# Kernel optimization log

Measured on AMD Instinct MI355X. Metric: run time of the kernel, lower is better.

Reference implementation:

```python
import jax, jax.numpy as jnp
import numpy as np

B, CIN, COUT, K, E, H, W = 32, 128, 256, 3, 8, 64, 64


def setup_inputs() -> dict:
    key = jax.random.key(0)
    k1, k2, k3, k4 = jax.random.split(key, 4)
    x = jax.random.normal(k1, (B, CIN, H, W), dtype=jnp.float32)
    expert_weight = jax.random.normal(k2, (E, COUT, CIN, K, K), dtype=jnp.float32)
    # nn.Linear(in_channels, num_experts): weight [E, CIN], bias [E]
    bound = 1.0 / np.sqrt(CIN)
    routing_w = jax.random.uniform(k3, (E, CIN), minval=-bound, maxval=bound, dtype=jnp.float32)
    routing_b = jax.random.uniform(k4, (E,), minval=-bound, maxval=bound, dtype=jnp.float32)
    return {"x": x, "expert_weight": expert_weight, "routing_w": routing_w, "routing_b": routing_b}


def reference(x, expert_weight, routing_w, routing_b):
    # routing: global-avg-pool -> linear -> softmax over experts
    pooled = x.mean(axis=(2, 3))                             # [B, CIN]
    logits = pooled @ routing_w.T + routing_b                # [B, E]
    rweights = jax.nn.softmax(logits, axis=-1)               # [B, E]
    # per-sample combined conv weights: [B, COUT, CIN, K, K]
    cw = jnp.einsum('be,eoikl->boikl', rweights, expert_weight)

    def conv_one(xi, wi):
        # xi: [CIN, H, W], wi: [COUT, CIN, K, K]; VALID conv, stride 1
        return jax.lax.conv_general_dilated(
            xi[None], wi, window_strides=(1, 1), padding='VALID',
            dimension_numbers=('NCHW', 'OIHW', 'NCHW'))[0]

    return jax.vmap(conv_one)(x, cw)                         # [B, COUT, H-K+1, W-K+1]
```

## Files before the change

### kernel.cpp

```cpp
#include <hip/hip_runtime.h>
#include <hip/hip_bf16.h>


#define CC_B    32
#define CC_CIN  128
#define CC_COUT 256
#define CC_NP   3844
#define CC_NT   18

typedef __attribute__((ext_vector_type(8))) short bf16x8;
typedef __attribute__((ext_vector_type(4))) float f32x4;

__global__ void cc_nhwc(const float* __restrict__ x, __hip_bfloat16* __restrict__ xn,
                        float* __restrict__ psum) {
    const int b = blockIdx.x >> 6, y = blockIdx.x & 63;
    __shared__ float lds[64 * 129];
    __shared__ float sred[256];
    const int t = threadIdx.x;
    const float* src = x + (size_t)b * CC_CIN * 4096 + y * 64;
#pragma unroll
    for (int i = 0; i < 32; ++i) {
        const int idx = i * 256 + t;
        const int cin = idx >> 6, xx = idx & 63;
        lds[xx * 129 + cin] = src[(size_t)cin * 4096 + xx];
    }
    __syncthreads();
    __hip_bfloat16* dst = xn + ((size_t)b * 4096 + y * 64) * CC_CIN;
#pragma unroll
    for (int j = 0; j < 4; ++j) {
        const int cidx = j * 256 + t;
        const int xx = cidx >> 4, c8 = (cidx & 15) * 8;
        union { __hip_bfloat16 h[8]; uint4 v; } u;
#pragma unroll
        for (int jj = 0; jj < 8; ++jj) u.h[jj] = __float2bfloat16(lds[xx * 129 + c8 + jj]);
        *reinterpret_cast<uint4*>(dst + (size_t)xx * CC_CIN + c8) = u.v;
    }
    const int cin = t & 127, xh = (t >> 7) * 32;
    float s = 0.f;
#pragma unroll
    for (int xx = 0; xx < 32; ++xx) s += lds[(xh + xx) * 129 + cin];
    sred[t] = s;
    __syncthreads();
    if (t < 128) psum[((size_t)b * 64 + y) * CC_CIN + t] = sred[t] + sred[t + 128];
}

__global__ void cc_route(const float* __restrict__ psum,
                         const float* __restrict__ rw_w,
                         const float* __restrict__ rw_b,
                         float* __restrict__ rweights) {
    const int b = blockIdx.x, c = threadIdx.x;
    __shared__ float pl[128];
    __shared__ float lg[8];
    const float* p = psum + (size_t)b * 64 * CC_CIN + c;
    float s = 0.f;
#pragma unroll 8
    for (int y = 0; y < 64; ++y) s += p[(size_t)y * CC_CIN];
    pl[c] = s * (1.f / 4096.f);
    __syncthreads();
    if (c < 8) {
        const float* w = rw_w + c * CC_CIN;
        float a = rw_b[c];
#pragma unroll 8
        for (int i = 0; i < CC_CIN; ++i) a += pl[i] * w[i];
        lg[c] = a;
    }
    __syncthreads();
    if (c == 0) {
        float m = lg[0];
#pragma unroll
        for (int e = 1; e < 8; ++e) m = fmaxf(m, lg[e]);
        float ex[8], sm = 0.f;
#pragma unroll
        for (int e = 0; e < 8; ++e) { ex[e] = __expf(lg[e] - m); sm += ex[e]; }
#pragma unroll
        for (int e = 0; e < 8; ++e) rweights[b * 8 + e] = ex[e] / sm;
    }
}

__global__ void cc_combine(const float* __restrict__ ew,
                           const float* __restrict__ rw,
                           __hip_bfloat16* __restrict__ cw) {
    const int t9 = blockIdx.x >> 8;
    const int cout = blockIdx.x & 255;
    const int cin = threadIdx.x;
    __shared__ float rws[256];
    rws[cin] = rw[cin];
    rws[cin + 128] = rw[cin + 128];
    __syncthreads();
    float wv[8];
    const size_t base = ((size_t)cout * CC_CIN + cin) * 9 + t9;
#pragma unroll
    for (int e = 0; e < 8; ++e) wv[e] = ew[base + (size_t)e * (CC_COUT * CC_CIN * 9)];
#pragma unroll 4
    for (int b = 0; b < CC_B; ++b) {
        float acc = 0.f;
#pragma unroll
        for (int e = 0; e < 8; ++e) acc += rws[b * 8 + e] * wv[e];
        cw[(((size_t)b * 9 + t9) * CC_COUT + cout) * CC_CIN + cin] = __float2bfloat16(acc);
    }
}

__device__ __forceinline__ void gload_lds16(const void* g, void* l) {
    __builtin_amdgcn_global_load_lds(
        (const __attribute__((address_space(1))) unsigned int*)g,
        (__attribute__((address_space(3))) unsigned int*)l, 16, 0, 0);
}

__global__ __launch_bounds__(512, 1) void cc_conv(
    const __hip_bfloat16* __restrict__ xn,
    const __hip_bfloat16* __restrict__ cw,
    float* __restrict__ out)
{
    __shared__ __align__(16) char smem[131072];
    const int l   = blockIdx.x;
    const int xcd = l & 7, li = l >> 3;
    const int b   = 4 * xcd + (li >> 5);
    const int r2  = li & 31;
    const int nt  = r2 >> 1, mt = r2 & 1;
    const int m0  = mt * 128;
    const int n0  = nt * 248;
    const int y0  = nt * 4;

    const int tid = threadIdx.x;
    const int wid = tid >> 6, lane = tid & 63;
    const int waveM = wid >> 2, waveN = wid & 3;

    f32x4 acc[4][4];
#pragma unroll
    for (int i = 0; i < 4; ++i)
#pragma unroll
        for (int j = 0; j < 4; ++j) acc[i][j] = (f32x4){0.f, 0.f, 0.f, 0.f};

    const int gsw = (lane & 7) ^ (lane >> 3);
    const __hip_bfloat16* cwb = cw + (size_t)b * 9 * CC_COUT * CC_CIN;
    const __hip_bfloat16* xnb = xn + (size_t)b * 4096 * CC_CIN;

    char* Bres = smem + 32768;
#pragma unroll
    for (int i = 0; i < 12; ++i) {
        const int idx = i * 8 + wid;
        const int h = idx / 48, rem = idx - h * 48;
        const int yy = rem >> 3, xb = rem & 7;
        const int x = xb * 8 + (lane >> 3);
        int yin = y0 + yy; if (yin > 63) yin = 63;
        gload_lds16(xnb + ((size_t)yin * 64 + x) * CC_CIN + h * 64 + gsw * 8,
                    Bres + idx * 1024);
    }

    int laOff[2];
#pragma unroll
    for (int i = 0; i < 2; ++i) {
        const int row = wid * 16 + i * 8 + (lane >> 3);
        laOff[i] = (m0 + row) * CC_CIN + gsw * 8;
    }
    auto stageA = [&](int t) {
        const int t9 = t >> 1;
        const int aoff = t9 * (CC_COUT * CC_CIN) + (t & 1) * 64;
        char* Ab = smem + (t & 1) * 16384 + wid * 2048;
#pragma unroll
        for (int i = 0; i < 2; ++i)
            gload_lds16(cwb + aoff + laOff[i], Ab + i * 1024);
    };
    stageA(0);
    stageA(1);

    const int rl = lane & 15, q = lane >> 4;
    int oyl[4], oxl[4];
#pragma unroll
    for (int nf = 0; nf < 4; ++nf) {
        int c = waveN * 64 + nf * 16 + rl;
        if (c > 247) c = 247;
        const int oy = c / 62;
        oyl[nf] = oy;
        oxl[nf] = c - 62 * oy;
    }

#pragma unroll 1
    for (int t = 0; t < CC_NT; ++t) {
        const char* Ab = smem + (t & 1) * 16384;
        const int t9 = t >> 1;
        const int ky = (t9 * 11) >> 5;
        const int kx = t9 - ky * 3;
        const int h = t & 1;

        if (t < CC_NT - 1) asm volatile("s_waitcnt vmcnt(2)" ::: "memory");
        else               asm volatile("s_waitcnt vmcnt(0)" ::: "memory");
        asm volatile("s_barrier" ::: "memory");

        bf16x8 af[8], bf[8];
#pragma unroll
        for (int mf = 0; mf < 4; ++mf)
#pragma unroll
            for (int kk = 0; kk < 2; ++kk) {
                const int r = waveM * 64 + mf * 16 + rl;
                af[mf * 2 + kk] = *(const bf16x8*)(Ab + r * 128 + (((kk * 4 + q) ^ (r & 7)) * 16));
            }
#pragma unroll
        for (int nf = 0; nf < 4; ++nf) {
            const int x = oxl[nf] + kx;
            const int row = (h * 6 + oyl[nf] + ky) * 64 + x;
#pragma unroll
            for (int kk = 0; kk < 2; ++kk)
                bf[nf * 2 + kk] = *(const bf16x8*)(Bres + row * 128 + (((kk * 4 + q) ^ (x & 7)) * 16));
        }
#pragma unroll
        for (int kk = 0; kk < 2; ++kk)
#pragma unroll
            for (int mf = 0; mf < 4; ++mf)
#pragma unroll
                for (int nf = 0; nf < 4; ++nf)
                    acc[mf][nf] = __builtin_amdgcn_mfma_f32_16x16x32_bf16(
                        af[mf * 2 + kk], bf[nf * 2 + kk], acc[mf][nf], 0, 0, 0);

        asm volatile("s_waitcnt lgkmcnt(0)" ::: "memory");
        asm volatile("s_barrier" ::: "memory");
        if (t + 2 < CC_NT) stageA(t + 2);
    }

    const int q4 = (lane >> 4) * 4;
#pragma unroll
    for (int mf = 0; mf < 4; ++mf) {
        const int crow = m0 + waveM * 64 + mf * 16 + q4;
#pragma unroll
        for (int nf = 0; nf < 4; ++nf) {
            const int c = waveN * 64 + nf * 16 + (lane & 15);
            const int p = n0 + c;
            if (c < 248 && p < CC_NP) {
                const size_t ob = ((size_t)b * CC_COUT + crow) * CC_NP + p;
#pragma unroll
                for (int j = 0; j < 4; ++j) out[ob + (size_t)j * CC_NP] = acc[mf][nf][j];
            }
        }
    }
}

extern "C" void kernel_launch(void* const* d_in, const int* in_sizes, int n_in,
                              void* d_out, int out_size, void* d_ws, size_t ws_size,
                              hipStream_t stream) {
    const float* x   = (const float*)d_in[0];
    const float* ew  = (const float*)d_in[1];
    const float* rww = (const float*)d_in[2];
    const float* rwb = (const float*)d_in[3];
    float* out = (float*)d_out;
    char* ws = (char*)d_ws;

    __hip_bfloat16* xnhwc = (__hip_bfloat16*)ws;
    __hip_bfloat16* cwcmb = (__hip_bfloat16*)(ws + 33554432);
    float* psum   = (float*)(ws + 52428800);
    float* rwts   = (float*)(ws + 53493760);

    cc_nhwc<<<dim3(CC_B * 64), dim3(256), 0, stream>>>(x, xnhwc, psum);
    cc_route<<<dim3(CC_B), dim3(128), 0, stream>>>(psum, rww, rwb, rwts);
    cc_combine<<<dim3(9 * CC_COUT), dim3(128), 0, stream>>>(ew, rwts, cwcmb);
    cc_conv<<<dim3(1024), dim3(512), 0, stream>>>(xnhwc, cwcmb, out);
}
```

Baseline: 129.8 us.

## Use 4-wave conv blocks with 2 blocks/CU and split-K input staging

Halves the conv block to 256 threads, with each wave computing a 64x128 tile (8 N-fragments) so two blocks fit per CU. The loop order is reordered so the first 9 steps cover channel half 0 and the last 9 cover half 1. This lets the input tile for each channel half be staged separately into a smaller LDS buffer (48KB instead of 96KB). It also fully unrolls the K loop and raises wave priority around the MFMA block. The aim is better latency hiding through two co-resident blocks, at the cost of higher register pressure from 128 accumulators per lane and a bigger unrolled body.

```diff
diff --git a/kernel.cpp b/kernel.cpp
--- a/kernel.cpp
+++ b/kernel.cpp
@@ -106,12 +106,12 @@
         (__attribute__((address_space(3))) unsigned int*)l, 16, 0, 0);
 }
 
-__global__ __launch_bounds__(512, 1) void cc_conv(
+__global__ __launch_bounds__(256, 2) void cc_conv(
     const __hip_bfloat16* __restrict__ xn,
     const __hip_bfloat16* __restrict__ cw,
     float* __restrict__ out)
 {
-    __shared__ __align__(16) char smem[131072];
+    __shared__ __align__(16) char smem[81920];
     const int l   = blockIdx.x;
     const int xcd = l & 7, li = l >> 3;
     const int b   = 4 * xcd + (li >> 5);
@@ -123,71 +123,73 @@
 
     const int tid = threadIdx.x;
     const int wid = tid >> 6, lane = tid & 63;
-    const int waveM = wid >> 2, waveN = wid & 3;
-
-    f32x4 acc[4][4];
+    const int waveM = wid >> 1, waveN = wid & 1;
+
+    f32x4 acc[4][8];
 #pragma unroll
     for (int i = 0; i < 4; ++i)
 #pragma unroll
-        for (int j = 0; j < 4; ++j) acc[i][j] = (f32x4){0.f, 0.f, 0.f, 0.f};
+        for (int j = 0; j < 8; ++j) acc[i][j] = (f32x4){0.f, 0.f, 0.f, 0.f};
 
     const int gsw = (lane & 7) ^ (lane >> 3);
     const __hip_bfloat16* cwb = cw + (size_t)b * 9 * CC_COUT * CC_CIN;
     const __hip_bfloat16* xnb = xn + (size_t)b * 4096 * CC_CIN;
 
-    char* Bres = smem + 32768;
-#pragma unroll
-    for (int i = 0; i < 12; ++i) {
-        const int idx = i * 8 + wid;
-        const int h = idx / 48, rem = idx - h * 48;
-        const int yy = rem >> 3, xb = rem & 7;
-        const int x = xb * 8 + (lane >> 3);
-        int yin = y0 + yy; if (yin > 63) yin = 63;
-        gload_lds16(xnb + ((size_t)yin * 64 + x) * CC_CIN + h * 64 + gsw * 8,
-                    Bres + idx * 1024);
-    }
-
-    int laOff[2];
-#pragma unroll
-    for (int i = 0; i < 2; ++i) {
-        const int row = wid * 16 + i * 8 + (lane >> 3);
+    int laOff[4];
+#pragma unroll
+    for (int i = 0; i < 4; ++i) {
+        const int row = wid * 32 + i * 8 + (lane >> 3);
         laOff[i] = (m0 + row) * CC_CIN + gsw * 8;
     }
     auto stageA = [&](int t) {
-        const int t9 = t >> 1;
-        const int aoff = t9 * (CC_COUT * CC_CIN) + (t & 1) * 64;
-        char* Ab = smem + (t & 1) * 16384 + wid * 2048;
-#pragma unroll
-        for (int i = 0; i < 2; ++i)
+        const int h = t / 9, t9 = t - 9 * h;
+        const int aoff = t9 * (CC_COUT * CC_CIN) + h * 64;
+        char* Ab = smem + (t & 1) * 16384 + wid * 4096;
+#pragma unroll
+        for (int i = 0; i < 4; ++i)
             gload_lds16(cwb + aoff + laOff[i], Ab + i * 1024);
     };
+
+    char* Bres = smem + 32768;
+    auto stageB = [&](int h) {
+#pragma unroll
+        for (int i = 0; i < 12; ++i) {
+            const int row = i * 32 + wid * 8 + (lane >> 3);
+            const int yy = row >> 6, x = row & 63;
+            int yin = y0 + yy; if (yin > 63) yin = 63;
+            gload_lds16(xnb + ((size_t)yin * 64 + x) * CC_CIN + h * 64 + gsw * 8,
+                        Bres + i * 4096 + wid * 1024);
+        }
+    };
+
+    const int rl = lane & 15, q = lane >> 4;
+
+    int oyl[8], oxl[8];
+#pragma unroll
+    for (int nf = 0; nf < 8; ++nf) {
+        int c = waveN * 128 + nf * 16 + rl;
+        int p = n0 + c; if (p > CC_NP - 1) p = CC_NP - 1;
+        if (c > 247) { p = n0 + 247; if (p > CC_NP - 1) p = CC_NP - 1; }
+        const int oy = p / 62;
+        oyl[nf] = oy - y0;
+        oxl[nf] = p - 62 * oy;
+    }
+
+    stageB(0);
     stageA(0);
     stageA(1);
 
-    const int rl = lane & 15, q = lane >> 4;
-    int oyl[4], oxl[4];
-#pragma unroll
-    for (int nf = 0; nf < 4; ++nf) {
-        int c = waveN * 64 + nf * 16 + rl;
-        if (c > 247) c = 247;
-        const int oy = c / 62;
-        oyl[nf] = oy;
-        oxl[nf] = c - 62 * oy;
-    }
-
-#pragma unroll 1
+#pragma unroll
     for (int t = 0; t < CC_NT; ++t) {
+        const int h = t / 9, t9 = t - 9 * h;
+        const int ky = t9 / 3, kx = t9 - 3 * ky;
         const char* Ab = smem + (t & 1) * 16384;
-        const int t9 = t >> 1;
-        const int ky = (t9 * 11) >> 5;
-        const int kx = t9 - ky * 3;
-        const int h = t & 1;
-
-        if (t < CC_NT - 1) asm volatile("s_waitcnt vmcnt(2)" ::: "memory");
+
+        if (t < CC_NT - 1) asm volatile("s_waitcnt vmcnt(4)" ::: "memory");
         else               asm volatile("s_waitcnt vmcnt(0)" ::: "memory");
         asm volatile("s_barrier" ::: "memory");
 
-        bf16x8 af[8], bf[8];
+        bf16x8 af[8], bf[16];
 #pragma unroll
         for (int mf = 0; mf < 4; ++mf)
 #pragma unroll
@@ -196,24 +198,27 @@
                 af[mf * 2 + kk] = *(const bf16x8*)(Ab + r * 128 + (((kk * 4 + q) ^ (r & 7)) * 16));
             }
 #pragma unroll
-        for (int nf = 0; nf < 4; ++nf) {
+        for (int nf = 0; nf < 8; ++nf) {
             const int x = oxl[nf] + kx;
-            const int row = (h * 6 + oyl[nf] + ky) * 64 + x;
+            const int row = (oyl[nf] + ky) * 64 + x;
 #pragma unroll
             for (int kk = 0; kk < 2; ++kk)
                 bf[nf * 2 + kk] = *(const bf16x8*)(Bres + row * 128 + (((kk * 4 + q) ^ (x & 7)) * 16));
         }
+        __builtin_amdgcn_s_setprio(1);
 #pragma unroll
         for (int kk = 0; kk < 2; ++kk)
 #pragma unroll
             for (int mf = 0; mf < 4; ++mf)
 #pragma unroll
-                for (int nf = 0; nf < 4; ++nf)
+                for (int nf = 0; nf < 8; ++nf)
                     acc[mf][nf] = __builtin_amdgcn_mfma_f32_16x16x32_bf16(
                         af[mf * 2 + kk], bf[nf * 2 + kk], acc[mf][nf], 0, 0, 0);
+        __builtin_amdgcn_s_setprio(0);
 
         asm volatile("s_waitcnt lgkmcnt(0)" ::: "memory");
         asm volatile("s_barrier" ::: "memory");
+        if (t == 8) stageB(1);
         if (t + 2 < CC_NT) stageA(t + 2);
     }
 
@@ -222,8 +227,8 @@
     for (int mf = 0; mf < 4; ++mf) {
         const int crow = m0 + waveM * 64 + mf * 16 + q4;
 #pragma unroll
-        for (int nf = 0; nf < 4; ++nf) {
-            const int c = waveN * 64 + nf * 16 + (lane & 15);
+        for (int nf = 0; nf < 8; ++nf) {
+            const int c = waveN * 128 + nf * 16 + (lane & 15);
             const int p = n0 + c;
             if (c < 248 && p < CC_NP) {
                 const size_t ob = ((size_t)b * CC_COUT + crow) * CC_NP + p;
@@ -252,5 +257,5 @@
     cc_nhwc<<<dim3(CC_B * 64), dim3(256), 0, stream>>>(x, xnhwc, psum);
     cc_route<<<dim3(CC_B), dim3(128), 0, stream>>>(psum, rww, rwb, rwts);
     cc_combine<<<dim3(9 * CC_COUT), dim3(128), 0, stream>>>(ew, rwts, cwcmb);
-    cc_conv<<<dim3(1024), dim3(512), 0, stream>>>(xnhwc, cwcmb, out);
-}
+    cc_conv<<<dim3(1024), dim3(256), 0, stream>>>(xnhwc, cwcmb, out);
+}
```

After: 186.7 us. +43.8%, slower.

## Halve resident input tile, reorder K loop by channel half, map waves to rows

Applied to the files above, without the earlier changes.

The conv kernel now keeps only one 64-channel half of the input tile in LDS at a time, cutting shared memory from 128KB to 80KB so more than one block can fit per CU. The half is reloaded mid-loop, after the first 9 taps, and the tap loop is reordered so the channel half is the outer index. Each wave now covers one output row of 62 pixels, which removes the per-lane divide and makes the swizzle follow the pixel row. The loop is also fully unrolled, per-kk fragment registers are narrowed, and MFMA blocks are wrapped in s_setprio. The cost is an extra synchronized reload of the input tile mid-loop and two wasted columns per wave.

```diff
diff --git a/kernel.cpp b/kernel.cpp
--- a/kernel.cpp
+++ b/kernel.cpp
@@ -106,12 +106,12 @@
         (__attribute__((address_space(3))) unsigned int*)l, 16, 0, 0);
 }
 
-__global__ __launch_bounds__(512, 1) void cc_conv(
+__global__ __launch_bounds__(512, 4) void cc_conv(
     const __hip_bfloat16* __restrict__ xn,
     const __hip_bfloat16* __restrict__ cw,
     float* __restrict__ out)
 {
-    __shared__ __align__(16) char smem[131072];
+    __shared__ __align__(16) char smem[81920];
     const int l   = blockIdx.x;
     const int xcd = l & 7, li = l >> 3;
     const int b   = 4 * xcd + (li >> 5);
@@ -119,7 +119,7 @@
     const int nt  = r2 >> 1, mt = r2 & 1;
     const int m0  = mt * 128;
     const int n0  = nt * 248;
-    const int y0  = nt * 4;
+    const int y0  = 4 * nt;
 
     const int tid = threadIdx.x;
     const int wid = tid >> 6, lane = tid & 63;
@@ -135,18 +135,6 @@
     const __hip_bfloat16* cwb = cw + (size_t)b * 9 * CC_COUT * CC_CIN;
     const __hip_bfloat16* xnb = xn + (size_t)b * 4096 * CC_CIN;
 
-    char* Bres = smem + 32768;
-#pragma unroll
-    for (int i = 0; i < 12; ++i) {
-        const int idx = i * 8 + wid;
-        const int h = idx / 48, rem = idx - h * 48;
-        const int yy = rem >> 3, xb = rem & 7;
-        const int x = xb * 8 + (lane >> 3);
-        int yin = y0 + yy; if (yin > 63) yin = 63;
-        gload_lds16(xnb + ((size_t)yin * 64 + x) * CC_CIN + h * 64 + gsw * 8,
-                    Bres + idx * 1024);
-    }
-
     int laOff[2];
 #pragma unroll
     for (int i = 0; i < 2; ++i) {
@@ -154,66 +142,75 @@
         laOff[i] = (m0 + row) * CC_CIN + gsw * 8;
     }
     auto stageA = [&](int t) {
-        const int t9 = t >> 1;
-        const int aoff = t9 * (CC_COUT * CC_CIN) + (t & 1) * 64;
+        const int h = t / 9, t9 = t - 9 * h;
+        const int aoff = t9 * (CC_COUT * CC_CIN) + h * 64;
         char* Ab = smem + (t & 1) * 16384 + wid * 2048;
 #pragma unroll
         for (int i = 0; i < 2; ++i)
             gload_lds16(cwb + aoff + laOff[i], Ab + i * 1024);
     };
+
+    char* Bres = smem + 32768;
+    const int bx = wid * 8 + (lane >> 3);
+    auto stageB = [&](int h) {
+#pragma unroll
+        for (int i = 0; i < 6; ++i) {
+            int yin = y0 + i; if (yin > 63) yin = 63;
+            gload_lds16(xnb + ((size_t)yin * 64 + bx) * CC_CIN + h * 64 + gsw * 8,
+                        Bres + i * 8192 + wid * 1024);
+        }
+    };
+
+    const int rl = lane & 15, q = lane >> 4;
+
+    int pixB[4];
+#pragma unroll
+    for (int nf = 0; nf < 4; ++nf) {
+        int c = nf * 16 + rl;
+        if (c > 61) c = 61;
+        pixB[nf] = waveN * 64 + c;
+    }
+
+    stageB(0);
     stageA(0);
     stageA(1);
 
-    const int rl = lane & 15, q = lane >> 4;
-    int oyl[4], oxl[4];
-#pragma unroll
-    for (int nf = 0; nf < 4; ++nf) {
-        int c = waveN * 64 + nf * 16 + rl;
-        if (c > 247) c = 247;
-        const int oy = c / 62;
-        oyl[nf] = oy;
-        oxl[nf] = c - 62 * oy;
-    }
-
-#pragma unroll 1
+#pragma unroll
     for (int t = 0; t < CC_NT; ++t) {
+        const int h = t / 9, t9 = t - 9 * h;
+        const int kyx = (t9 / 3) * 64 + (t9 - 3 * (t9 / 3));
         const char* Ab = smem + (t & 1) * 16384;
-        const int t9 = t >> 1;
-        const int ky = (t9 * 11) >> 5;
-        const int kx = t9 - ky * 3;
-        const int h = t & 1;
 
         if (t < CC_NT - 1) asm volatile("s_waitcnt vmcnt(2)" ::: "memory");
         else               asm volatile("s_waitcnt vmcnt(0)" ::: "memory");
         asm volatile("s_barrier" ::: "memory");
 
-        bf16x8 af[8], bf[8];
-#pragma unroll
-        for (int mf = 0; mf < 4; ++mf)
-#pragma unroll
-            for (int kk = 0; kk < 2; ++kk) {
+#pragma unroll
+        for (int kk = 0; kk < 2; ++kk) {
+            bf16x8 af[4], bf[4];
+#pragma unroll
+            for (int mf = 0; mf < 4; ++mf) {
                 const int r = waveM * 64 + mf * 16 + rl;
-                af[mf * 2 + kk] = *(const bf16x8*)(Ab + r * 128 + (((kk * 4 + q) ^ (r & 7)) * 16));
+                af[mf] = *(const bf16x8*)(Ab + r * 128 + (((kk * 4 + q) ^ (r & 7)) * 16));
             }
 #pragma unroll
-        for (int nf = 0; nf < 4; ++nf) {
-            const int x = oxl[nf] + kx;
-            const int row = (h * 6 + oyl[nf] + ky) * 64 + x;
-#pragma unroll
-            for (int kk = 0; kk < 2; ++kk)
-                bf[nf * 2 + kk] = *(const bf16x8*)(Bres + row * 128 + (((kk * 4 + q) ^ (x & 7)) * 16));
-        }
-#pragma unroll
-        for (int kk = 0; kk < 2; ++kk)
+            for (int nf = 0; nf < 4; ++nf) {
+                const int row = pixB[nf] + kyx;
+                bf[nf] = *(const bf16x8*)(Bres + row * 128 + (((kk * 4 + q) ^ (row & 7)) * 16));
+            }
+            __builtin_amdgcn_s_setprio(1);
 #pragma unroll
             for (int mf = 0; mf < 4; ++mf)
 #pragma unroll
                 for (int nf = 0; nf < 4; ++nf)
                     acc[mf][nf] = __builtin_amdgcn_mfma_f32_16x16x32_bf16(
-                        af[mf * 2 + kk], bf[nf * 2 + kk], acc[mf][nf], 0, 0, 0);
+                        af[mf], bf[nf], acc[mf][nf], 0, 0, 0);
+            __builtin_amdgcn_s_setprio(0);
+        }
 
         asm volatile("s_waitcnt lgkmcnt(0)" ::: "memory");
         asm volatile("s_barrier" ::: "memory");
+        if (t == 8) stageB(1);
         if (t + 2 < CC_NT) stageA(t + 2);
     }
 
@@ -223,9 +220,9 @@
         const int crow = m0 + waveM * 64 + mf * 16 + q4;
 #pragma unroll
         for (int nf = 0; nf < 4; ++nf) {
-            const int c = waveN * 64 + nf * 16 + (lane & 15);
-            const int p = n0 + c;
-            if (c < 248 && p < CC_NP) {
+            const int c = nf * 16 + (lane & 15);
+            const int p = n0 + waveN * 62 + c;
+            if (c < 62 && p < CC_NP) {
                 const size_t ob = ((size_t)b * CC_COUT + crow) * CC_NP + p;
 #pragma unroll
                 for (int j = 0; j < 4; ++j) out[ob + (size_t)j * CC_NP] = acc[mf][nf][j];
```

Result: slower. 156.4 us (+20.5%).
